# Performance work log

Measured on AMD Instinct MI355X. Metric: run time of the kernel, lower is better.

## Reference

```python
import jax, jax.numpy as jnp
import numpy as np

N = 50000        # nodes
E = 1_600_000    # edges
F = 32           # in/out channels
T = 4            # towers
FT = F // T      # per-tower channels = 8
ED = 16          # edge_dim
L = 5            # num PNA layers


def setup_inputs() -> dict:
    key = jax.random.key(0)
    ks = jax.random.split(key, 11)
    s = 0.2  # weight scale
    return {
        "x": jax.random.normal(ks[0], (N, F), jnp.float32),
        "edge_index": jax.random.randint(ks[1], (2, E), 0, N, dtype=jnp.int32),
        "edge_attr": jax.random.normal(ks[2], (E, ED), jnp.float32),
        # per-layer stacked PNAConv parameters
        "edge_W": jax.random.normal(ks[3], (L, ED, FT), jnp.float32) * s,
        "edge_b": jax.random.normal(ks[4], (L, FT), jnp.float32) * s,
        "pre_W": jax.random.normal(ks[5], (L, T, 3 * FT, FT), jnp.float32) * s,
        "pre_b": jax.random.normal(ks[6], (L, T, FT), jnp.float32) * s,
        "post_W": jax.random.normal(ks[7], (L, T, 4 * FT, FT), jnp.float32) * s,
        "post_b": jax.random.normal(ks[8], (L, T, FT), jnp.float32) * s,
        "lin_W": jax.random.normal(ks[9], (L, T * FT, F), jnp.float32) * s,
        "lin_b": jax.random.normal(ks[10], (L, F), jnp.float32) * s,
    }


def _pna_layer(x, src, dst, edge_attr, eW, eb, pW, pb, poW, pob, lW, lb):
    n = x.shape[0]
    xt = x.reshape(n, T, FT)                       # divide_input=True
    ee = edge_attr @ eW + eb                       # [E, FT], shared edge encoder
    xi = xt[dst]                                   # target node features [E, T, FT]
    xj = xt[src]                                   # source node features [E, T, FT]
    ee_b = jnp.broadcast_to(ee[:, None, :], (ee.shape[0], T, FT))
    h = jnp.concatenate([xi, xj, ee_b], axis=-1)   # [E, T, 3*FT]
    # per-tower pre-MLP (pre_layers=1)
    h = jnp.einsum('etk,tkf->etf', h, pW) + pb     # [E, T, FT]
    # aggregators: mean, sum, max (scaler = identity)
    ssum = jax.ops.segment_sum(h, dst, num_segments=n)
    cnt = jax.ops.segment_sum(jnp.ones((h.shape[0],), h.dtype), dst, num_segments=n)
    mean = ssum / jnp.maximum(cnt, 1.0)[:, None, None]
    mx = jax.ops.segment_max(h, dst, num_segments=n)
    mx = jnp.where(cnt[:, None, None] > 0, mx, 0.0)  # empty segments -> 0 (PyG convention)
    out = jnp.concatenate([xt, mean, ssum, mx], axis=-1)  # [N, T, 4*FT]
    # per-tower post-MLP (post_layers=1)
    out = jnp.einsum('ntk,tkf->ntf', out, poW) + pob      # [N, T, FT]
    out = out.reshape(n, T * FT) @ lW + lb                # final mixing linear
    return jax.nn.relu(out)


def reference(x, edge_index, edge_attr, edge_W, edge_b, pre_W, pre_b,
              post_W, post_b, lin_W, lin_b):
    src, dst = edge_index[0], edge_index[1]
    for l in range(L):
        x = _pna_layer(x, src, dst, edge_attr,
                       edge_W[l], edge_b[l], pre_W[l], pre_b[l],
                       post_W[l], post_b[l], lin_W[l], lin_b[l])
    return x
```

## Files before the change

kernel.cpp:

```cpp
#include <hip/hip_runtime.h>
#include <hip/hip_fp16.h>

#define NN 50000
#define NE 1600000
#define F 32
#define T 4
#define FT 8
#define ED 16
#define NLAYERS 5

typedef _Float16 h2 __attribute__((ext_vector_type(2)));

__device__ __forceinline__ float dot2(h2 a, h2 b, float c) {
#if __has_builtin(__builtin_amdgcn_fdot2)
    return __builtin_amdgcn_fdot2(a, b, c, false);
#else
    return c + (float)a.x * (float)b.x + (float)a.y * (float)b.y;
#endif
}


__global__ void zero_cnt(int* __restrict__ cnt) {
    int i = blockIdx.x * 256 + threadIdx.x;
    if (i < NN) cnt[i] = 0;
}

__global__ void count_kernel(const int* __restrict__ ei, int* __restrict__ cnt) {
    int e = blockIdx.x * 256 + threadIdx.x;
    if (e >= NE) return;
    atomicAdd(&cnt[ei[NE + e]], 1);
}

__global__ void scan_kernel(const int* __restrict__ cnt, int* __restrict__ row_ptr,
                            int* __restrict__ cursor) {
    __shared__ int wsum[16];
    __shared__ int carry_s;
    int tid = threadIdx.x;
    int lane = tid & 63, wid = tid >> 6;
    if (tid == 0) carry_s = 0;
    __syncthreads();
    for (int base = 0; base < NN; base += 1024) {
        int i = base + tid;
        int v = (i < NN) ? cnt[i] : 0;
        int s = v;
#pragma unroll
        for (int off = 1; off < 64; off <<= 1) {
            int tt = __shfl_up(s, off, 64);
            if (lane >= off) s += tt;
        }
        __syncthreads();
        if (lane == 63) wsum[wid] = s;
        __syncthreads();
        if (wid == 0 && lane < 16) {
            int w = wsum[lane];
            int ws = w;
#pragma unroll
            for (int off = 1; off < 16; off <<= 1) {
                int tt = __shfl_up(ws, off, 16);
                if (lane >= off) ws += tt;
            }
            wsum[lane] = ws - w;
        }
        __syncthreads();
        int excl = carry_s + wsum[wid] + s - v;
        if (i < NN) { row_ptr[i] = excl; cursor[i] = excl; }
        __syncthreads();
        if (tid == 1023) carry_s += wsum[15] + s;
    }
}

__global__ void build_kernel(const int* __restrict__ ei,
                             const float* __restrict__ eattr,
                             int* __restrict__ cursor,
                             int* __restrict__ src_s,
                             float4* __restrict__ eh) {
    int e = blockIdx.x * 256 + threadIdx.x;
    if (e >= NE) return;
    int src = ei[e];
    int dst = ei[NE + e];
    const float4* eap = (const float4*)(eattr + (size_t)e * ED);
    float4 v0 = eap[0], v1 = eap[1], v2 = eap[2], v3 = eap[3];
    union { __half hh[16]; float4 f4[2]; } u;
    u.hh[0]  = __float2half(v0.x); u.hh[1]  = __float2half(v0.y);
    u.hh[2]  = __float2half(v0.z); u.hh[3]  = __float2half(v0.w);
    u.hh[4]  = __float2half(v1.x); u.hh[5]  = __float2half(v1.y);
    u.hh[6]  = __float2half(v1.z); u.hh[7]  = __float2half(v1.w);
    u.hh[8]  = __float2half(v2.x); u.hh[9]  = __float2half(v2.y);
    u.hh[10] = __float2half(v2.z); u.hh[11] = __float2half(v2.w);
    u.hh[12] = __float2half(v3.x); u.hh[13] = __float2half(v3.y);
    u.hh[14] = __float2half(v3.z); u.hh[15] = __float2half(v3.w);
    int p = atomicAdd(&cursor[dst], 1);
    src_s[p] = src << 5;
    eh[2 * (size_t)p]     = u.f4[0];
    eh[2 * (size_t)p + 1] = u.f4[1];
}

__global__ void layer_const(const float* __restrict__ edge_W,
                            const float* __restrict__ edge_b,
                            const float* __restrict__ pre_W,
                            const float* __restrict__ pre_b,
                            float4* __restrict__ wchp,
                            float* __restrict__ abias) {
    int idx = threadIdx.x;
    if (idx >= NLAYERS * 32) return;
    int l = idx >> 5, ch = idx & 31;
    int t = ch >> 3, f = ch & 7;
    const float* eW = edge_W + (size_t)l * ED * FT;
    const float* eb = edge_b + (size_t)l * FT;
    const float* pW = pre_W + (size_t)l * T * 24 * FT;
    const float* pb = pre_b + (size_t)l * T * FT;
    float pj[8];
#pragma unroll
    for (int j = 0; j < 8; j++) pj[j] = pW[(t * 24 + 16 + j) * 8 + f];
    union { _Float16 hh[16]; float4 f4[2]; } u;
#pragma unroll
    for (int k = 0; k < 16; k++) {
        float s = 0.f;
#pragma unroll
        for (int j = 0; j < 8; j++) s += eW[k * 8 + j] * pj[j];
        u.hh[k] = (_Float16)s;
    }
    float c0 = pb[t * 8 + f];
#pragma unroll
    for (int j = 0; j < 8; j++) c0 += eb[j] * pj[j];
    wchp[2 * idx]     = u.f4[0];
    wchp[2 * idx + 1] = u.f4[1];
    abias[idx] = c0;
}


__device__ __forceinline__ unsigned short f2bf_rne(float v) {
    unsigned u = __float_as_uint(v);
    return (unsigned short)((u + 0x7FFFu + ((u >> 16) & 1u)) >> 16);
}

__global__ void node_pre(const float* __restrict__ xin,
                         const float* __restrict__ preW,
                         unsigned short* __restrict__ b16) {
    int idx = blockIdx.x * 256 + threadIdx.x;
    if (idx >= NN * F) return;
    int n = idx >> 5, ch = idx & 31;
    int t = ch >> 3, f = ch & 7;
    const float* xrow = xin + n * F + t * FT;
    const float* wB = preW + (t * 24 + 8) * 8 + f;
    float bv = 0.f;
#pragma unroll
    for (int k = 0; k < 8; k++) bv += xrow[k] * wB[k * 8];
    b16[idx] = f2bf_rne(bv);
}

__global__ __launch_bounds__(256) void gather_post(
        const float* __restrict__ xin,
        const unsigned short* __restrict__ b16_in,
        unsigned short* __restrict__ b16_out,
        const float4* __restrict__ eh,
        const int* __restrict__ row_ptr, const int* __restrict__ cnt,
        const int* __restrict__ src_s,
        const float4* __restrict__ wchp_l,
        const float* __restrict__ abias_l,
        const float* __restrict__ preW,
        const float* __restrict__ postW, const float* __restrict__ postb,
        const float* __restrict__ linW, const float* __restrict__ linb,
        const float* __restrict__ preW_next,
        float* __restrict__ xout) {
    __shared__ float smS[4][32];
    __shared__ float smM[4][32];
    int tid = threadIdx.x;
    int wv = tid >> 6;
    int lane = tid & 63;
    int n = blockIdx.x * 4 + wv;

    int chgrp = lane >> 3;
    int e_sub = lane & 7;

    union { float4 f4[8]; h2 p[32]; } uw;
#pragma unroll
    for (int c = 0; c < 4; c++) {
        uw.f4[2 * c]     = wchp_l[2 * (chgrp * 4 + c)];
        uw.f4[2 * c + 1] = wchp_l[2 * (chgrp * 4 + c) + 1];
    }

    int rs = row_ptr[n], deg = cnt[n];
    int re = rs + deg;

    float S[4] = {0.f, 0.f, 0.f, 0.f};
    float M[4] = {-3.4e38f, -3.4e38f, -3.4e38f, -3.4e38f};
    for (int i = rs + e_sub; i < re; i += 8) {
        int s = src_s[i];
        float4 lo = eh[2 * (size_t)i];
        float4 hi = eh[2 * (size_t)i + 1];
        ushort4 b4 = *(const ushort4*)(b16_in + s + chgrp * 4);
        unsigned short bv[4] = {b4.x, b4.y, b4.z, b4.w};
        union { float4 f4; h2 p[4]; } ua, ub;
        ua.f4 = lo; ub.f4 = hi;
#pragma unroll
        for (int c = 0; c < 4; c++) {
            float h = __uint_as_float((unsigned)bv[c] << 16);
            h = dot2(ua.p[0], uw.p[c * 8 + 0], h);
            h = dot2(ua.p[1], uw.p[c * 8 + 1], h);
            h = dot2(ua.p[2], uw.p[c * 8 + 2], h);
            h = dot2(ua.p[3], uw.p[c * 8 + 3], h);
            h = dot2(ub.p[0], uw.p[c * 8 + 4], h);
            h = dot2(ub.p[1], uw.p[c * 8 + 5], h);
            h = dot2(ub.p[2], uw.p[c * 8 + 6], h);
            h = dot2(ub.p[3], uw.p[c * 8 + 7], h);
            S[c] += h;
            M[c] = fmaxf(M[c], h);
        }
    }
#pragma unroll
    for (int m = 1; m < 8; m <<= 1) {
#pragma unroll
        for (int c = 0; c < 4; c++) {
            S[c] += __shfl_xor(S[c], m, 64);
            M[c] = fmaxf(M[c], __shfl_xor(M[c], m, 64));
        }
    }
    if (e_sub == 0) {
#pragma unroll
        for (int c = 0; c < 4; c++) {
            smS[wv][chgrp * 4 + c] = S[c];
            smM[wv][chgrp * 4 + c] = M[c];
        }
    }
    __syncthreads();

    int ch = lane & 31, half = lane >> 5;
    int t = ch >> 3, f = ch & 7;
    float Sc = smS[wv][ch];
    float Mc = smM[wv][ch];

    float xv = xin[(size_t)n * F + ch];
    float a_val = abias_l[ch];
#pragma unroll
    for (int j = 0; j < 8; j++)
        a_val += __shfl(xv, t * 8 + j, 64) * preW[(t * 24 + j) * 8 + f];

    float sum_h, mean_h, max_h;
    if (deg > 0) {
        sum_h = Sc + (float)deg * a_val;
        mean_h = sum_h / (float)deg;
        max_h = Mc + a_val;
    } else {
        sum_h = 0.f; mean_h = 0.f; max_h = 0.f;
    }

    float ua0 = 0.f, ua1 = 0.f, ua2 = 0.f, ua3 = 0.f;
#pragma unroll
    for (int kk = 0; kk < 8; kk++) {
        int sl = t * 8 + kk;
        ua0 += __shfl(xv,     sl, 64) * postW[(t * 32 + 0 * 8 + kk) * 8 + f];
        ua1 += __shfl(mean_h, sl, 64) * postW[(t * 32 + 1 * 8 + kk) * 8 + f];
        ua2 += __shfl(sum_h,  sl, 64) * postW[(t * 32 + 2 * 8 + kk) * 8 + f];
        ua3 += __shfl(max_h,  sl, 64) * postW[(t * 32 + 3 * 8 + kk) * 8 + f];
    }
    float u2 = postb[t * 8 + f] + ((ua0 + ua1) + (ua2 + ua3));

    float y0 = 0.f, y1 = 0.f, y2 = 0.f, y3 = 0.f;
#pragma unroll
    for (int k = 0; k < 8; k++) {
        y0 += __shfl(u2, k,      64) * linW[k * 32 + ch];
        y1 += __shfl(u2, 8 + k,  64) * linW[(8 + k) * 32 + ch];
        y2 += __shfl(u2, 16 + k, 64) * linW[(16 + k) * 32 + ch];
        y3 += __shfl(u2, 24 + k, 64) * linW[(24 + k) * 32 + ch];
    }
    float y = linb[ch] + ((y0 + y1) + (y2 + y3));
    y = fmaxf(y, 0.f);
    if (half == 0)
        xout[(size_t)n * F + ch] = y;

    if (preW_next) {
        float bn = 0.f;
#pragma unroll
        for (int j = 0; j < 8; j++)
            bn += __shfl(y, t * 8 + j, 64) * preW_next[(t * 24 + 8 + j) * 8 + f];
        if (half == 0)
            b16_out[(size_t)n * F + ch] = f2bf_rne(bn);
    }
}


extern "C" void kernel_launch(void* const* d_in, const int* in_sizes, int n_in,
                              void* d_out, int out_size, void* d_ws, size_t ws_size,
                              hipStream_t stream) {
    const float* x      = (const float*)d_in[0];
    const int*   ei     = (const int*)d_in[1];
    const float* eattr  = (const float*)d_in[2];
    const float* edge_W = (const float*)d_in[3];
    const float* edge_b = (const float*)d_in[4];
    const float* pre_W  = (const float*)d_in[5];
    const float* pre_b  = (const float*)d_in[6];
    const float* post_W = (const float*)d_in[7];
    const float* post_b = (const float*)d_in[8];
    const float* lin_W  = (const float*)d_in[9];
    const float* lin_b  = (const float*)d_in[10];
    float* out = (float*)d_out;

    const size_t NC = (size_t)NN * F;
    char* p = (char*)d_ws;
    float4* eh    = (float4*)p;        p += sizeof(float4) * 2 * (size_t)NE;
    int* src_s    = (int*)p;           p += sizeof(int) * NE;
    int* cnt      = (int*)p;           p += sizeof(int) * NN;
    int* row_ptr  = (int*)p;           p += sizeof(int) * NN;
    int* cursor   = (int*)p;           p += sizeof(int) * NN;
    unsigned short* b16a = (unsigned short*)p;  p += sizeof(unsigned short) * NC;
    unsigned short* b16b = (unsigned short*)p;  p += sizeof(unsigned short) * NC;
    float* xb0    = (float*)p;         p += sizeof(float) * NC;
    float* xb1    = (float*)p;         p += sizeof(float) * NC;
    float4* wchp  = (float4*)p;        p += sizeof(float4) * 2 * NLAYERS * 32;
    float* abias  = (float*)p;         p += sizeof(float) * NLAYERS * 32;

    dim3 blk(256);
    int gN  = (NN + 255) / 256;
    int gE  = (NE + 255) / 256;
    int gNC = (NN * F + 255) / 256;
    int gG  = NN / 4;

    hipLaunchKernelGGL(zero_cnt,     dim3(gN), blk, 0, stream, cnt);
    hipLaunchKernelGGL(count_kernel, dim3(gE), blk, 0, stream, ei, cnt);
    hipLaunchKernelGGL(scan_kernel,  dim3(1), dim3(1024), 0, stream, cnt, row_ptr, cursor);
    hipLaunchKernelGGL(build_kernel, dim3(gE), blk, 0, stream, ei, eattr,
                       cursor, src_s, eh);
    hipLaunchKernelGGL(layer_const,  dim3(1), blk, 0, stream,
                       edge_W, edge_b, pre_W, pre_b, wchp, abias);

    hipLaunchKernelGGL(node_pre, dim3(gNC), blk, 0, stream, x, pre_W, b16a);

    const float* xin = x;
    for (int l = 0; l < NLAYERS; l++) {
        const float* pW  = pre_W  + (size_t)l * T * 24 * FT;
        const float* poW = post_W + (size_t)l * T * 32 * FT;
        const float* pob = post_b + (size_t)l * T * FT;
        const float* lW  = lin_W  + (size_t)l * F * F;
        const float* lb  = lin_b  + (size_t)l * F;
        const float* pWn = (l + 1 < NLAYERS) ? (pre_W + (size_t)(l + 1) * T * 24 * FT)
                                             : nullptr;
        float* xout = (l == NLAYERS - 1) ? out : ((l & 1) ? xb1 : xb0);
        const unsigned short* bin  = (l & 1) ? b16b : b16a;
        unsigned short*       bout = (l & 1) ? b16a : b16b;

        hipLaunchKernelGGL(gather_post, dim3(gG), blk, 0, stream,
                           xin, bin, pWn ? bout : nullptr, eh, row_ptr, cnt, src_s,
                           wchp + (size_t)l * 64, abias + (size_t)l * 32,
                           pW, poW, pob, lW, lb, pWn, xout);
        xin = xout;
    }
}
```

Measured before the change: 722.2 us.

## Stage edge features and source indices through LDS with async global-to-LDS loads

After: 744.9 us. +3.1%, slower.

```diff
diff --git a/kernel.cpp b/kernel.cpp
--- a/kernel.cpp
+++ b/kernel.cpp
@@ -18,6 +18,20 @@
     return c + (float)a.x * (float)b.x + (float)a.y * (float)b.y;
 #endif
 }
+
+#if __has_builtin(__builtin_amdgcn_global_load_lds)
+#define HAS_GLDS 1
+__device__ __forceinline__ void glds16(const void* g, void* l) {
+    __builtin_amdgcn_global_load_lds(
+        (const __attribute__((address_space(1))) unsigned*)g,
+        (__attribute__((address_space(3))) unsigned*)l, 16, 0, 0);
+}
+__device__ __forceinline__ void glds4(const void* g, void* l) {
+    __builtin_amdgcn_global_load_lds(
+        (const __attribute__((address_space(1))) unsigned*)g,
+        (__attribute__((address_space(3))) unsigned*)l, 4, 0, 0);
+}
+#endif
 
 
 __global__ void zero_cnt(int* __restrict__ cnt) {
@@ -163,6 +177,7 @@
         const float* __restrict__ linW, const float* __restrict__ linb,
         const float* __restrict__ preW_next,
         float* __restrict__ xout) {
+    __shared__ __align__(16) char stage[4][2304];
     __shared__ float smS[4][32];
     __shared__ float smM[4][32];
     int tid = threadIdx.x;
@@ -172,6 +187,7 @@
 
     int chgrp = lane >> 3;
     int e_sub = lane & 7;
+    const unsigned short* bp = b16_in + chgrp * 4;
 
     union { float4 f4[8]; h2 p[32]; } uw;
 #pragma unroll
@@ -182,30 +198,56 @@
 
     int rs = row_ptr[n], deg = cnt[n];
     int re = rs + deg;
+    float xv = xin[(size_t)n * F + (lane & 31)];
+
+    char* ehbuf = stage[wv];
+    const int* srcbuf = (const int*)(stage[wv] + 2048);
 
     float S[4] = {0.f, 0.f, 0.f, 0.f};
     float M[4] = {-3.4e38f, -3.4e38f, -3.4e38f, -3.4e38f};
-    for (int i = rs + e_sub; i < re; i += 8) {
-        int s = src_s[i];
-        float4 lo = eh[2 * (size_t)i];
-        float4 hi = eh[2 * (size_t)i + 1];
-        ushort4 b4 = *(const ushort4*)(b16_in + s + chgrp * 4);
-        unsigned short bv[4] = {b4.x, b4.y, b4.z, b4.w};
-        union { float4 f4; h2 p[4]; } ua, ub;
-        ua.f4 = lo; ub.f4 = hi;
-#pragma unroll
-        for (int c = 0; c < 4; c++) {
-            float h = __uint_as_float((unsigned)bv[c] << 16);
-            h = dot2(ua.p[0], uw.p[c * 8 + 0], h);
-            h = dot2(ua.p[1], uw.p[c * 8 + 1], h);
-            h = dot2(ua.p[2], uw.p[c * 8 + 2], h);
-            h = dot2(ua.p[3], uw.p[c * 8 + 3], h);
-            h = dot2(ub.p[0], uw.p[c * 8 + 4], h);
-            h = dot2(ub.p[1], uw.p[c * 8 + 5], h);
-            h = dot2(ub.p[2], uw.p[c * 8 + 6], h);
-            h = dot2(ub.p[3], uw.p[c * 8 + 7], h);
-            S[c] += h;
-            M[c] = fmaxf(M[c], h);
+    const unsigned MAXS = (NN - 1) * F;
+
+    for (int base = rs; base < re; base += 64) {
+        const char* ehb = (const char*)(eh + 2 * (size_t)base);
+#ifdef HAS_GLDS
+        glds16(ehb + lane * 16, ehbuf);
+        glds16(ehb + 1024 + lane * 16, ehbuf + 1024);
+        glds4((const char*)(src_s + base) + lane * 4, (void*)srcbuf);
+        asm volatile("s_waitcnt vmcnt(0)" ::: "memory");
+#else
+        *(float4*)(ehbuf + lane * 16) = *(const float4*)(ehb + lane * 16);
+        *(float4*)(ehbuf + 1024 + lane * 16) = *(const float4*)(ehb + 1024 + lane * 16);
+        ((int*)srcbuf)[lane] = src_s[base + lane];
+#endif
+        ushort4 bk[8];
+#pragma unroll
+        for (int k = 0; k < 8; k++) {
+            unsigned s = (unsigned)srcbuf[e_sub + 8 * k];
+            if (s > MAXS) s = 0;
+            bk[k] = *(const ushort4*)(bp + s);
+        }
+#pragma unroll
+        for (int k = 0; k < 8; k++) {
+            int j = e_sub + 8 * k;
+            bool valid = (base + j) < re;
+            union { float4 f4; h2 p[4]; } ua, ub;
+            ua.f4 = *(const float4*)(ehbuf + j * 32);
+            ub.f4 = *(const float4*)(ehbuf + j * 32 + 16);
+            unsigned short bvv[4] = {bk[k].x, bk[k].y, bk[k].z, bk[k].w};
+#pragma unroll
+            for (int c = 0; c < 4; c++) {
+                float h = __uint_as_float((unsigned)bvv[c] << 16);
+                h = dot2(ua.p[0], uw.p[c * 8 + 0], h);
+                h = dot2(ua.p[1], uw.p[c * 8 + 1], h);
+                h = dot2(ua.p[2], uw.p[c * 8 + 2], h);
+                h = dot2(ua.p[3], uw.p[c * 8 + 3], h);
+                h = dot2(ub.p[0], uw.p[c * 8 + 4], h);
+                h = dot2(ub.p[1], uw.p[c * 8 + 5], h);
+                h = dot2(ub.p[2], uw.p[c * 8 + 6], h);
+                h = dot2(ub.p[3], uw.p[c * 8 + 7], h);
+                S[c] += valid ? h : 0.f;
+                M[c] = valid ? fmaxf(M[c], h) : M[c];
+            }
         }
     }
 #pragma unroll
@@ -230,7 +272,6 @@
     float Sc = smS[wv][ch];
     float Mc = smM[wv][ch];
 
-    float xv = xin[(size_t)n * F + ch];
     float a_val = abias_l[ch];
 #pragma unroll
     for (int j = 0; j < 8; j++)
```
